# Performance work log

Measured on AMD Instinct MI355X. Metric: run time of the kernel, lower is better.

## Reference

```python
import jax, jax.numpy as jnp
import numpy as np

NUM_HEADS = 16

def setup_inputs() -> dict:
    key = jax.random.key(0)
    ks = jax.random.split(key, 5)
    N, T, D = 16, 4096, 1024
    # Linear weights stored as (in, out): y = x @ W + b (equivalent to torch x @ W.T + b)
    return {
        "x": jax.random.normal(ks[0], (N, T, D), jnp.float32),
        "w_qkv": jax.random.normal(ks[1], (D, 3 * D), jnp.float32) * (D ** -0.5),
        "b_qkv": jax.random.normal(ks[2], (3 * D,), jnp.float32) * 0.02,
        "w_proj": jax.random.normal(ks[3], (D, D), jnp.float32) * (D ** -0.5),
        "b_proj": jax.random.normal(ks[4], (D,), jnp.float32) * 0.02,
    }

def reference(x, w_qkv, b_qkv, w_proj, b_proj):
    N, T, D = x.shape
    H = NUM_HEADS
    hd = D // H
    scale = hd ** -0.5
    qkv = x @ w_qkv + b_qkv                      # (N,T,3D)
    qkv = qkv.reshape(N, T, 3, H, hd)
    q, k, v = qkv[:, :, 0], qkv[:, :, 1], qkv[:, :, 2]   # each (N,T,H,hd)
    # Faithful to source: matmul over last two dims -> scores across HEADS, (N,T,H,H)
    attn = jnp.einsum('nthd,ntgd->nthg', q * scale, k)
    attn = jax.nn.softmax(attn, axis=-1)
    out = jnp.einsum('nthg,ntgd->nthd', attn, v)         # (N,T,H,hd)
    # Faithful: transpose(2,1) then flatten -> (N,H,T,hd).reshape(N,T,D)
    out = out.transpose(0, 2, 1, 3).reshape(N, T, D)
    return out @ w_proj + b_proj
```

## Files before the change

kernel.cpp:

```cpp
#include <hip/hip_runtime.h>
#include <hip/hip_bf16.h>
#include <stdint.h>

typedef __bf16 bf16x8 __attribute__((ext_vector_type(8)));
typedef float f32x4 __attribute__((ext_vector_type(4)));
typedef unsigned short us8 __attribute__((ext_vector_type(8)));

__device__ __forceinline__ float bf2f(unsigned short u) {
    return __uint_as_float(((unsigned)u) << 16);
}
__device__ __forceinline__ unsigned short f2bf(float f) {
    __bf16 b = (__bf16)f;
    return __builtin_bit_cast(unsigned short, b);
}

__device__ __forceinline__ void gload16(const char* g, char* l) {
    __builtin_amdgcn_global_load_lds(
        (const __attribute__((address_space(1))) void*)g,
        (__attribute__((address_space(3))) void*)l, 16, 0, 0);
}

__global__ __launch_bounds__(256) void transpose_cast(
    const float* __restrict__ in, unsigned short* __restrict__ out,
    int K, int N)
{
    __shared__ float tile[32][33];
    const int tx = threadIdx.x, ty = threadIdx.y;
    const int n0 = blockIdx.x * 32, k0 = blockIdx.y * 32;
    #pragma unroll
    for (int i = 0; i < 32; i += 8)
        tile[ty + i][tx] = in[(long)(k0 + ty + i) * N + n0 + tx];
    __syncthreads();
    #pragma unroll
    for (int i = 0; i < 32; i += 8)
        out[(long)(n0 + ty + i) * K + k0 + tx] = f2bf(tile[tx][ty + i]);
}

__global__ __launch_bounds__(256) void cast_f32_bf16(
    const float* __restrict__ in, unsigned short* __restrict__ out, long n)
{
    const long stride = (long)gridDim.x * 256 * 8;
    for (long i = ((long)blockIdx.x * 256 + threadIdx.x) * 8; i < n; i += stride) {
        const f32x4 u0 = *(const f32x4*)&in[i];
        const f32x4 u1 = *(const f32x4*)&in[i + 4];
        us8 w;
        #pragma unroll
        for (int e = 0; e < 4; ++e) { w[e] = f2bf(u0[e]); w[e + 4] = f2bf(u1[e]); }
        *(us8*)&out[i] = w;
    }
}

#define MFMA16x16(a, b, c) __builtin_amdgcn_mfma_f32_16x16x32_bf16(a, b, c, 0, 0, 0)
#define BAR __builtin_amdgcn_s_barrier()
#define SB  __builtin_amdgcn_sched_barrier(0)
#define P1_ __builtin_amdgcn_s_setprio(1);
#define P0_ __builtin_amdgcn_s_setprio(0);

#define MFMA16(AA, BB, RO)                                                     \
    _Pragma("unroll") for (int mi_ = 0; mi_ < 4; ++mi_)                        \
        _Pragma("unroll") for (int ni_ = 0; ni_ < 4; ++ni_)                    \
            acc[(RO)+mi_][ni_] =                                               \
                MFMA16x16(AA[mi_], BB[ni_], acc[(RO)+mi_][ni_]);

#define RD_A4(DST, BUFOFF, HIOFF, KS)                                          \
    _Pragma("unroll") for (int mi_ = 0; mi_ < 4; ++mi_)                        \
        DST[mi_] = *(const bf16x8*)(smem + (BUFOFF) + aBase + (HIOFF) + mi_*2048 + (KS));

#define RD_B4(DST, BUFOFF, KS)                                                 \
    _Pragma("unroll") for (int ni_ = 0; ni_ < 4; ++ni_)                        \
        DST[ni_] = *(const bf16x8*)(smem + (BUFOFF) + bBase + ni_*2048 + (KS));

#define TILE4(T_, BUF, OBUF, SG, SR)                                           \
  do {                                                                         \
    const long gk = (long)((T_) + 2) * 128;                                    \
                          \
    RD_A4(AH0, BUF, 8192, k0)                                                  \
    SB; asm volatile("s_waitcnt lgkmcnt(4)"); SB;                              \
    P1_ MFMA16(AL0, B0, 0) P0_                                                 \
                                           \
    RD_A4(AL1, BUF, 0, k1)                                                     \
    RD_B4(B1, BUF, k1)                                                         \
    SB; asm volatile("s_waitcnt lgkmcnt(8)"); SB;                              \
    P1_ MFMA16(AH0, B0, 4) P0_                                                 \
           \
    BAR;                                                                       \
    RD_A4(AH1, BUF, 8192, k1)                                                  \
    if (SG) {                                                                  \
        gload16(aStage + (long)(0*64)*Kb + gk, smem + (BUF) + 0*8192 + ldsW);  \
        gload16(aStage + (long)(2*64)*Kb + gk, smem + (BUF) + 2*8192 + ldsW);  \
        gload16(bStage + (long)(0*64)*Kb + gk, smem + (BUF) + 32768 + 0*8192 + ldsW); \
        gload16(bStage + (long)(1*64)*Kb + gk, smem + (BUF) + 32768 + 1*8192 + ldsW); \
    }                                                                          \
    SB; asm volatile("s_waitcnt lgkmcnt(4)"); SB;                              \
    P1_ MFMA16(AL1, B1, 0) P0_                                                 \
    SB;                                                                        \
    if (SG) asm volatile("s_waitcnt vmcnt(4)");                                \
    else    asm volatile("s_waitcnt vmcnt(0)");                                \
    SB;                                                                        \
      \
    BAR;                                                                       \
    if (SR) { RD_A4(AL0, OBUF, 0, k0) RD_B4(B0, OBUF, k0) }                    \
    if (SG) {                                                                  \
        gload16(aStage + (long)(1*64)*Kb + gk, smem + (BUF) + 1*8192 + ldsW);  \
        gload16(aStage + (long)(3*64)*Kb + gk, smem + (BUF) + 3*8192 + ldsW);  \
        gload16(bStage + (long)(2*64)*Kb + gk, smem + (BUF) + 32768 + 2*8192 + ldsW); \
        gload16(bStage + (long)(3*64)*Kb + gk, smem + (BUF) + 32768 + 3*8192 + ldsW); \
    }                                                                          \
    SB;                                                                        \
    if (SR) asm volatile("s_waitcnt lgkmcnt(8)");                              \
    else    asm volatile("s_waitcnt lgkmcnt(0)");                              \
    SB;                                                                        \
    P1_ MFMA16(AH1, B1, 4) P0_                                                 \
  } while (0)

template<bool OUT_BF16>
__global__ __launch_bounds__(512, 2)
void gemm256(const unsigned short* __restrict__ A,
             const unsigned short* __restrict__ BT,
             const float* __restrict__ bias,
             void* __restrict__ Cp,
             int M, int N, int K)
{
    extern __shared__ char smem[];
    const int tid  = threadIdx.x;
    const int lane = tid & 63;
    const int w    = tid >> 6;
    const int wm   = w >> 2;
    const int wn   = w & 3;

    const int nwg  = gridDim.x;
    const int bid0 = blockIdx.x;
    const int bid  = (bid0 & 7) * (nwg >> 3) + (bid0 >> 3);
    const int nbx  = N >> 8;
    const int bx   = bid % nbx, by = bid / nbx;
    const long rowStart = (long)by * 256;
    const int  colStart = bx * 256;

    const long Kb = (long)K * 2;

    const int srow = w * 8 + (lane >> 3);
    const int scol = ((lane & 7) ^ (lane >> 3)) << 4;
    const char* aStage = (const char*)A  + (rowStart + srow) * Kb + scol;
    const char* bStage = (const char*)BT + ((long)colStart + srow) * Kb + scol;
    const int ldsW = w * 1024;

    const int fr = lane & 15;
    const int kq = lane >> 4;
    const int sw = (fr & 7) << 4;
    const int k0 = (kq * 16) ^ sw;
    const int k1 = (64 + kq * 16) ^ sw;
    const int aBase = (wm * 128 + fr) * 128;
    const int bBase = 32768 + (wn * 64 + fr) * 128;

    f32x4 acc[8][4] = {};
    bf16x8 AL0[4], AH0[4], AL1[4], AH1[4], B0[4], B1[4];

    #pragma unroll
    for (int tt = 0; tt < 2; ++tt) {
        #pragma unroll
        for (int j = 0; j < 4; ++j)
            gload16(aStage + (long)(j * 64) * Kb + (long)tt * 128,
                    smem + tt * 65536 + j * 8192 + ldsW);
        #pragma unroll
        for (int j = 0; j < 4; ++j)
            gload16(bStage + (long)(j * 64) * Kb + (long)tt * 128,
                    smem + tt * 65536 + 32768 + j * 8192 + ldsW);
    }
    asm volatile("s_waitcnt vmcnt(8)");
    BAR;
    RD_B4(B0, 0, k0)
    RD_A4(AL0, 0, 0, k0)

    #pragma unroll 1
    for (int tp = 0; tp < 7; ++tp) {
        TILE4(2 * tp,     0,     65536, 1, 1);
        TILE4(2 * tp + 1, 65536, 0,     1, 1);
    }
    TILE4(14, 0,     65536, 0, 1);
    TILE4(15, 65536, 0,     0, 0);

    float bv[4];
    #pragma unroll
    for (int ni = 0; ni < 4; ++ni)
        bv[ni] = bias[colStart + wn * 64 + ni * 16 + fr];
    #pragma unroll
    for (int mi = 0; mi < 8; ++mi) {
        #pragma unroll
        for (int ni = 0; ni < 4; ++ni) {
            const int col = colStart + wn * 64 + ni * 16 + fr;
            #pragma unroll
            for (int e = 0; e < 4; ++e) {
                const long row = rowStart + wm * 128 + mi * 16 + kq * 4 + e;
                const float val = acc[mi][ni][e] + bv[ni];
                if constexpr (OUT_BF16)
                    ((unsigned short*)Cp)[row * N + col] = f2bf(val);
                else
                    ((float*)Cp)[row * N + col] = val;
            }
        }
    }
}

__global__ __launch_bounds__(256) void attn_kernel(
    const unsigned short* __restrict__ qkv, unsigned short* __restrict__ out)
{
    __shared__ unsigned short qkvs[4][3072];
    __shared__ float ps[4][320];
    __shared__ unsigned short os[4][1024];
    const int tid = threadIdx.x, lane = tid & 63, wave = tid >> 6;
    const long blockTok = (long)blockIdx.x * 4;

    const unsigned short* src = qkv + blockTok * 3072;
    unsigned short* dstBase = &qkvs[0][0];
    #pragma unroll
    for (int i = 0; i < 6; ++i) {
        const int o = (i * 256 + tid) * 8;
        *(us8*)&dstBase[o] = *(const us8*)&src[o];
    }
    __syncthreads();

    const unsigned short* q  = &qkvs[wave][0];
    const unsigned short* kk = &qkvs[wave][1024];
    const unsigned short* vv = &qkvs[wave][2048];

    const int fr = lane & 15, kq = lane >> 4;
    const int fo = fr * 64 + kq * 8;
    const bf16x8 aq0 = *(const bf16x8*)&q[fo];
    const bf16x8 aq1 = *(const bf16x8*)&q[fo + 32];
    const bf16x8 bk0 = *(const bf16x8*)&kk[fo];
    const bf16x8 bk1 = *(const bf16x8*)&kk[fo + 32];
    f32x4 s = {};
    s = __builtin_amdgcn_mfma_f32_16x16x32_bf16(aq0, bk0, s, 0, 0, 0);
    s = __builtin_amdgcn_mfma_f32_16x16x32_bf16(aq1, bk1, s, 0, 0, 0);

    #pragma unroll
    for (int r = 0; r < 4; ++r) {
        const float v_ = s[r] * 0.125f;
        float m_ = v_;
        m_ = fmaxf(m_, __shfl_xor(m_, 1, 64));
        m_ = fmaxf(m_, __shfl_xor(m_, 2, 64));
        m_ = fmaxf(m_, __shfl_xor(m_, 4, 64));
        m_ = fmaxf(m_, __shfl_xor(m_, 8, 64));
        const float p_ = expf(v_ - m_);
        float t_ = p_;
        t_ += __shfl_xor(t_, 1, 64);
        t_ += __shfl_xor(t_, 2, 64);
        t_ += __shfl_xor(t_, 4, 64);
        t_ += __shfl_xor(t_, 8, 64);
        ps[wave][(kq * 4 + r) * 20 + fr] = p_ / t_;
    }
    __syncthreads();

    const int h = lane >> 2, db = lane & 3;
    float o16[16] = {};
    #pragma unroll
    for (int gq = 0; gq < 4; ++gq) {
        const f32x4 pv = *(const f32x4*)&ps[wave][h * 20 + gq * 4];
        #pragma unroll
        for (int j = 0; j < 4; ++j) {
            const float pg = pv[j];
            const int g = gq * 4 + j;
            const us8 v8a = *(const us8*)&vv[g * 64 + db * 16];
            const us8 v8b = *(const us8*)&vv[g * 64 + db * 16 + 8];
            #pragma unroll
            for (int e = 0; e < 8; ++e) {
                o16[e]     += pg * bf2f(v8a[e]);
                o16[8 + e] += pg * bf2f(v8b[e]);
            }
        }
    }
    us8 w0, w1;
    #pragma unroll
    for (int e = 0; e < 8; ++e) { w0[e] = f2bf(o16[e]); w1[e] = f2bf(o16[8 + e]); }
    *(us8*)&os[wave][h * 64 + db * 16] = w0;
    *(us8*)&os[wave][h * 64 + db * 16 + 8] = w1;
    __syncthreads();

    #pragma unroll
    for (int i = 0; i < 2; ++i) {
        const int c = i * 256 + tid;
        const int w2 = c >> 7;
        const int cc = c & 127;
        const long m = blockTok + w2;
        const long n_ = m >> 12;
        const int t = (int)(m & 4095);
        const int hh = cc >> 3, slot = cc & 7;
        const long row = n_ * 4096 + hh * 256 + (t >> 4);
        const long colb = (long)(t & 15) * 128 + slot * 16;
        *(us8*)((char*)out + row * 2048 + colb) = *(const us8*)&os[w2][cc * 8];
    }
}

extern "C" void kernel_launch(void* const* d_in, const int* in_sizes, int n_in,
                              void* d_out, int out_size, void* d_ws, size_t ws_size,
                              hipStream_t stream) {
    const float* x      = (const float*)d_in[0];
    const float* w_qkv  = (const float*)d_in[1];
    const float* b_qkv  = (const float*)d_in[2];
    const float* w_proj = (const float*)d_in[3];
    const float* b_proj = (const float*)d_in[4];

    const long M = 65536;
    const size_t QKV_B = (size_t)M * 3072 * 2;
    const size_t XB_B  = (size_t)M * 1024 * 2;
    const size_t WQ_B  = 3072 * 1024 * 2;
    const size_t WP_B  = 1024 * 1024 * 2;
    if (ws_size < QKV_B + XB_B + WQ_B + WP_B) return;

    char* ws = (char*)d_ws;
    unsigned short* qkv    = (unsigned short*)ws;
    unsigned short* xb     = (unsigned short*)(ws + QKV_B);
    unsigned short* wqkvT  = (unsigned short*)(ws + QKV_B + XB_B);
    unsigned short* wprojT = (unsigned short*)(ws + QKV_B + XB_B + WQ_B);

    hipFuncSetAttribute((const void*)gemm256<true>,
                        hipFuncAttributeMaxDynamicSharedMemorySize, 131072);
    hipFuncSetAttribute((const void*)gemm256<false>,
                        hipFuncAttributeMaxDynamicSharedMemorySize, 131072);

    dim3 tb(32, 8);
    transpose_cast<<<dim3(3072 / 32, 1024 / 32), tb, 0, stream>>>(w_qkv, wqkvT, 1024, 3072);
    transpose_cast<<<dim3(1024 / 32, 1024 / 32), tb, 0, stream>>>(w_proj, wprojT, 1024, 1024);
    cast_f32_bf16<<<2048, 256, 0, stream>>>(x, xb, M * 1024);

    gemm256<true><<<dim3((3072 / 256) * (M / 256)), 512, 131072, stream>>>(
        xb, wqkvT, b_qkv, qkv, (int)M, 3072, 1024);

    attn_kernel<<<dim3(M / 4), 256, 0, stream>>>(qkv, xb);

    gemm256<false><<<dim3((1024 / 256) * (M / 256)), 512, 131072, stream>>>(
        xb, wprojT, b_proj, d_out, (int)M, 1024, 1024);
}
```

Before: 739.5 us.

## Restructure GEMM main loop into four barrier-separated phases with split prefetch

Rewrites the double-buffered 256x256 GEMM inner tile into four phases, each loading its own A/B fragments from LDS, waiting for them with lgkmcnt(0), and issuing 16 MFMAs between block barriers. Global-to-LDS prefetches are split so two A chunks of the next tile go into the other buffer in phase one, and the rest of the tile after next go into the current buffer in the last phase. This drops register-level prefetch of the next tile's fragments, using fewer fragment registers. In exchange it adds barriers and full LDS waits that serialize LDS reads with MFMA work.

```diff
diff --git a/kernel.cpp b/kernel.cpp
--- a/kernel.cpp
+++ b/kernel.cpp
@@ -70,47 +70,46 @@
     _Pragma("unroll") for (int ni_ = 0; ni_ < 4; ++ni_)                        \
         DST[ni_] = *(const bf16x8*)(smem + (BUFOFF) + bBase + ni_*2048 + (KS));
 
-#define TILE4(T_, BUF, OBUF, SG, SR)                                           \
+#define TILE4C(T_, BUF, OBUF, SGP0, SGP3)                                      \
   do {                                                                         \
-    const long gk = (long)((T_) + 2) * 128;                                    \
-                          \
-    RD_A4(AH0, BUF, 8192, k0)                                                  \
-    SB; asm volatile("s_waitcnt lgkmcnt(4)"); SB;                              \
-    P1_ MFMA16(AL0, B0, 0) P0_                                                 \
-                                           \
-    RD_A4(AL1, BUF, 0, k1)                                                     \
+    const long gk1 = (long)((T_) + 1) * 128;                                   \
+    const long gk2 = (long)((T_) + 2) * 128;                                   \
+              \
+    RD_A4(Aa, BUF, 0, k0)                                                      \
+    RD_B4(B0, BUF, k0)                                                         \
+    if (SGP0) {                                                                \
+        gload16(aStage + (long)(1*64)*Kb + gk1, smem + (OBUF) + 1*8192 + ldsW);\
+        gload16(aStage + (long)(3*64)*Kb + gk1, smem + (OBUF) + 3*8192 + ldsW);\
+    }                                                                          \
+    BAR; asm volatile("s_waitcnt lgkmcnt(0)"); SB;                             \
+    P1_ MFMA16(Aa, B0, 0) P0_                                                  \
+    BAR;                                                                       \
+                                            \
+    RD_A4(Ab, BUF, 8192, k0)                                                   \
+    BAR; asm volatile("s_waitcnt lgkmcnt(0)"); SB;                             \
+    P1_ MFMA16(Ab, B0, 4) P0_                                                  \
+    BAR;                                                                       \
+                                     \
+    RD_A4(Aa, BUF, 0, k1)                                                      \
     RD_B4(B1, BUF, k1)                                                         \
-    SB; asm volatile("s_waitcnt lgkmcnt(8)"); SB;                              \
-    P1_ MFMA16(AH0, B0, 4) P0_                                                 \
-           \
+    BAR; asm volatile("s_waitcnt lgkmcnt(0)"); SB;                             \
+    P1_ MFMA16(Aa, B1, 0) P0_                                                  \
     BAR;                                                                       \
-    RD_A4(AH1, BUF, 8192, k1)                                                  \
-    if (SG) {                                                                  \
-        gload16(aStage + (long)(0*64)*Kb + gk, smem + (BUF) + 0*8192 + ldsW);  \
-        gload16(aStage + (long)(2*64)*Kb + gk, smem + (BUF) + 2*8192 + ldsW);  \
-        gload16(bStage + (long)(0*64)*Kb + gk, smem + (BUF) + 32768 + 0*8192 + ldsW); \
-        gload16(bStage + (long)(1*64)*Kb + gk, smem + (BUF) + 32768 + 1*8192 + ldsW); \
+          \
+    RD_A4(Ab, BUF, 8192, k1)                                                   \
+    if (SGP3) {                                                                \
+        gload16(aStage + (long)(0*64)*Kb + gk2, smem + (BUF) + 0*8192 + ldsW); \
+        gload16(aStage + (long)(2*64)*Kb + gk2, smem + (BUF) + 2*8192 + ldsW); \
+        _Pragma("unroll") for (int j = 0; j < 4; ++j)                          \
+            gload16(bStage + (long)(j*64)*Kb + gk2,                            \
+                    smem + (BUF) + 32768 + j*8192 + ldsW);                     \
+        SB; asm volatile("s_waitcnt vmcnt(6)"); SB;                            \
+    } else if (SGP0) {                                                         \
+        SB; asm volatile("s_waitcnt vmcnt(0)"); SB;                            \
     }                                                                          \
-    SB; asm volatile("s_waitcnt lgkmcnt(4)"); SB;                              \
-    P1_ MFMA16(AL1, B1, 0) P0_                                                 \
-    SB;                                                                        \
-    if (SG) asm volatile("s_waitcnt vmcnt(4)");                                \
-    else    asm volatile("s_waitcnt vmcnt(0)");                                \
-    SB;                                                                        \
-      \
+    BAR; asm volatile("s_waitcnt lgkmcnt(0)"); SB;                             \
+    P1_ MFMA16(Ab, B1, 4) P0_                                                  \
     BAR;                                                                       \
-    if (SR) { RD_A4(AL0, OBUF, 0, k0) RD_B4(B0, OBUF, k0) }                    \
-    if (SG) {                                                                  \
-        gload16(aStage + (long)(1*64)*Kb + gk, smem + (BUF) + 1*8192 + ldsW);  \
-        gload16(aStage + (long)(3*64)*Kb + gk, smem + (BUF) + 3*8192 + ldsW);  \
-        gload16(bStage + (long)(2*64)*Kb + gk, smem + (BUF) + 32768 + 2*8192 + ldsW); \
-        gload16(bStage + (long)(3*64)*Kb + gk, smem + (BUF) + 32768 + 3*8192 + ldsW); \
-    }                                                                          \
-    SB;                                                                        \
-    if (SR) asm volatile("s_waitcnt lgkmcnt(8)");                              \
-    else    asm volatile("s_waitcnt lgkmcnt(0)");                              \
-    SB;                                                                        \
-    P1_ MFMA16(AH1, B1, 4) P0_                                                 \
   } while (0)
 
 template<bool OUT_BF16>
@@ -153,31 +152,30 @@
     const int bBase = 32768 + (wn * 64 + fr) * 128;
 
     f32x4 acc[8][4] = {};
-    bf16x8 AL0[4], AH0[4], AL1[4], AH1[4], B0[4], B1[4];
-
-    #pragma unroll
-    for (int tt = 0; tt < 2; ++tt) {
-        #pragma unroll
-        for (int j = 0; j < 4; ++j)
-            gload16(aStage + (long)(j * 64) * Kb + (long)tt * 128,
-                    smem + tt * 65536 + j * 8192 + ldsW);
-        #pragma unroll
-        for (int j = 0; j < 4; ++j)
-            gload16(bStage + (long)(j * 64) * Kb + (long)tt * 128,
-                    smem + tt * 65536 + 32768 + j * 8192 + ldsW);
-    }
-    asm volatile("s_waitcnt vmcnt(8)");
+    bf16x8 Aa[4], Ab[4], B0[4], B1[4];
+
+    #pragma unroll
+    for (int j = 0; j < 4; ++j)
+        gload16(aStage + (long)(j * 64) * Kb, smem + j * 8192 + ldsW);
+    #pragma unroll
+    for (int j = 0; j < 4; ++j)
+        gload16(bStage + (long)(j * 64) * Kb, smem + 32768 + j * 8192 + ldsW);
+    gload16(aStage + (long)(0 * 64) * Kb + 128, smem + 65536 + 0 * 8192 + ldsW);
+    gload16(aStage + (long)(2 * 64) * Kb + 128, smem + 65536 + 2 * 8192 + ldsW);
+    #pragma unroll
+    for (int j = 0; j < 4; ++j)
+        gload16(bStage + (long)(j * 64) * Kb + 128,
+                smem + 65536 + 32768 + j * 8192 + ldsW);
+    SB; asm volatile("s_waitcnt vmcnt(6)"); SB;
     BAR;
-    RD_B4(B0, 0, k0)
-    RD_A4(AL0, 0, 0, k0)
 
     #pragma unroll 1
     for (int tp = 0; tp < 7; ++tp) {
-        TILE4(2 * tp,     0,     65536, 1, 1);
-        TILE4(2 * tp + 1, 65536, 0,     1, 1);
-    }
-    TILE4(14, 0,     65536, 0, 1);
-    TILE4(15, 65536, 0,     0, 0);
+        TILE4C(2 * tp,     0,     65536, 1, 1);
+        TILE4C(2 * tp + 1, 65536, 0,     1, 1);
+    }
+    TILE4C(14, 0,     65536, 1, 0);
+    TILE4C(15, 65536, 0,     0, 0);
 
     float bv[4];
     #pragma unroll
```

New measurement: 796.1 us. 1.08x slower.
